# Kernel optimization log

Hardware: AMD Instinct MI355X
Metric: run time of the kernel (lower is better)

Reference implementation:

```python
import jax, jax.numpy as jnp
import numpy as np

N, E, H, NIN, DD = 10000, 160000, 128, 128, 256
SCALE = 30.0
EPS = 1e-5

def _ln(x, g, b):
    mu = jnp.mean(x, axis=-1, keepdims=True)
    var = jnp.mean((x - mu) ** 2, axis=-1, keepdims=True)
    return (x - mu) * jax.lax.rsqrt(var + EPS) * g + b

def _gelu(x):
    return jax.nn.gelu(x, approximate=False)  # torch nn.GELU default (erf)

def setup_inputs() -> dict:
    key = jax.random.key(0)
    ks = jax.random.split(key, 16)
    def w(k, i, o):
        return jax.random.normal(k, (i, o), jnp.float32) * (1.0 / np.sqrt(i))
    return {
        "h_V": jax.random.normal(ks[0], (N, H), jnp.float32),
        "h_E": jax.random.normal(ks[1], (E, H + NIN), jnp.float32),
        "edge_idx": jax.random.randint(ks[2], (2, E), 0, N, jnp.int32),
        # message MLP: (H+NIN)->H, H->H
        "m_w0": w(ks[3], H + NIN, H), "m_b0": jnp.zeros((H,), jnp.float32),
        "m_w1": w(ks[4], H, H),       "m_b1": jnp.zeros((H,), jnp.float32),
        # dense MLP: H->DD, DD->DD, final DD->H
        "d_w0": w(ks[5], H, DD),  "d_b0": jnp.zeros((DD,), jnp.float32),
        "d_w1": w(ks[6], DD, DD), "d_b1": jnp.zeros((DD,), jnp.float32),
        "d_w2": w(ks[7], DD, H),  "d_b2": jnp.zeros((H,), jnp.float32),
        # LayerNorm params
        "g1": jnp.ones((H,), jnp.float32), "be1": jnp.zeros((H,), jnp.float32),
        "g2": jnp.ones((H,), jnp.float32), "be2": jnp.zeros((H,), jnp.float32),
    }

def reference(h_V, h_E, edge_idx, m_w0, m_b0, m_w1, m_b1,
              d_w0, d_b0, d_w1, d_b1, d_w2, d_b2, g1, be1, g2, be2):
    src_idx = edge_idx[0]
    # message MLP over edges (dropout = identity at inference)
    h = _gelu(h_E @ m_w0 + m_b0)
    h_message = _gelu(h @ m_w1 + m_b1)          # [E, H]
    # scatter-sum aggregate edges -> nodes
    dh = jax.ops.segment_sum(h_message, src_idx, num_segments=N) / SCALE
    h_V = _ln(h_V + dh, g1, be1)
    # dense MLP over nodes
    d = _gelu(h_V @ d_w0 + d_b0)
    d = _gelu(d @ d_w1 + d_b1)
    dh = d @ d_w2 + d_b2
    return _ln(h_V + dh, g2, be2)
```

## Files before the change

### kernel.cpp

```cpp
#include <hip/hip_runtime.h>
#include <hip/hip_bf16.h>


typedef __attribute__((ext_vector_type(8))) short bf16x8;
typedef __attribute__((ext_vector_type(4))) float f32x4;

__device__ __forceinline__ unsigned short f2bf(float f) {
  union { float f; unsigned u; } v; v.f = f;
  return (unsigned short)((v.u + 0x7fffu + ((v.u >> 16) & 1u)) >> 16);
}
__device__ __forceinline__ unsigned pk2bf(float a, float b) {
  __hip_bfloat162 h = __float22bfloat162_rn(make_float2(a, b));
  union { __hip_bfloat162 h; unsigned u; } v; v.h = h;
  return v.u;
}
__device__ __forceinline__ float bf2f(unsigned s) {
  union { unsigned u; float f; } v; v.u = s << 16;
  return v.f;
}
__device__ __forceinline__ float gelu_f(float x) {
  float u = x * 0.70710678118654752f;
  float au = fabsf(u);
  float t = __builtin_amdgcn_rcpf(1.0f + 0.3275911f * au);
  float poly = ((((1.061405429f * t - 1.453152027f) * t + 1.421413741f) * t -
                 0.284496736f) * t + 0.254829592f) * t;
  float e = __expf(-au * au);
  float erfu = copysignf(1.0f - poly * e, u);
  return 0.5f * x * (1.0f + erfu);
}

__global__ void k_pack(const float* __restrict__ mw0, const float* __restrict__ mw1,
                       const float* __restrict__ dw0, const float* __restrict__ dw1,
                       const float* __restrict__ dw2,
                       unsigned short* __restrict__ pw0, unsigned short* __restrict__ pw1,
                       unsigned short* __restrict__ pd0, unsigned short* __restrict__ pd1,
                       unsigned short* __restrict__ pd2) {
  int g = blockIdx.x, lane = threadIdx.x;
  const float* src; unsigned short* dst; int K, N, WC, base;
  if (g < 64)       { src = mw0; dst = pw0; K = 256; N = 128; WC = 32; base = 0; }
  else if (g < 96)  { src = mw1; dst = pw1; K = 128; N = 128; WC = 32; base = 64; }
  else if (g < 160) { src = dw0; dst = pd0; K = 128; N = 256; WC = 64; base = 96; }
  else if (g < 288) { src = dw1; dst = pd1; K = 256; N = 256; WC = 32; base = 160; }
  else              { src = dw2; dst = pd2; K = 256; N = 128; WC = 32; base = 288; }
  int lg = g - base;
  int KS = K >> 5, CTKS = (WC >> 4) * KS;
  int w = lg / CTKS, rem = lg % CTKS, ct = rem / KS, ks = rem % KS;
  int col = w * WC + ct * 16 + (lane & 15);
  int k0 = ks * 32 + (lane >> 4) * 8;
  unsigned short o[8];
#pragma unroll
  for (int j = 0; j < 8; ++j) o[j] = f2bf(src[(size_t)(k0 + j) * N + col]);
  uint4 u;
  u.x = (unsigned)o[0] | ((unsigned)o[1] << 16);
  u.y = (unsigned)o[2] | ((unsigned)o[3] << 16);
  u.z = (unsigned)o[4] | ((unsigned)o[5] << 16);
  u.w = (unsigned)o[6] | ((unsigned)o[7] << 16);
  *(uint4*)(dst + (size_t)(lg * 64 + lane) * 8) = u;
}

__global__ void k_hist(const int* __restrict__ eidx, int* __restrict__ counts, int E) {
  int e = blockIdx.x * 256 + threadIdx.x;
  if (e < E) atomicAdd(&counts[eidx[e]], 1);
}

__global__ __launch_bounds__(1024) void k_scan(const int* __restrict__ counts,
                                               int* __restrict__ row_start,
                                               int* __restrict__ cursor, int Nn) {
  __shared__ int sm[1024];
  int t = threadIdx.x;
  int chunk = (Nn + 1023) / 1024;
  int lo = t * chunk, hi = lo + chunk;
  if (hi > Nn) hi = Nn;
  int s = 0;
  for (int i = lo; i < hi; ++i) s += counts[i];
  sm[t] = s;
  __syncthreads();
  for (int o = 1; o < 1024; o <<= 1) {
    int u = (t >= o) ? sm[t - o] : 0;
    __syncthreads();
    sm[t] += u;
    __syncthreads();
  }
  int run = sm[t] - s;
  for (int i = lo; i < hi; ++i) {
    row_start[i] = run; cursor[i] = run; run += counts[i];
  }
  if (t == 1023) row_start[Nn] = sm[1023];
}

__global__ void k_scatter(const int* __restrict__ eidx, int* __restrict__ cursor,
                          int* __restrict__ eorder, int E) {
  int e = blockIdx.x * 256 + threadIdx.x;
  if (e < E) {
    int pos = atomicAdd(&cursor[eidx[e]], 1);
    eorder[pos] = e;
  }
}

__global__ __launch_bounds__(256, 3) void k_edge(
    const float* __restrict__ hE, const unsigned short* __restrict__ pw0,
    const unsigned short* __restrict__ pw1, const float* __restrict__ b0,
    const float* __restrict__ b1, unsigned short* __restrict__ hmsg, int E) {
  __shared__ __align__(16) char ldsA[64 * 512];
  const int tid = threadIdx.x;
  const int wid = tid >> 6, lane = tid & 63;
  const int l15 = lane & 15, lhi = lane >> 4;
  const int wcol = wid * 32;

  bf16x8 B0[16], B1[8];
  {
    const uint4* p0 = (const uint4*)pw0 + (size_t)(wid * 16) * 64 + lane;
#pragma unroll
    for (int f = 0; f < 16; ++f) { uint4 v = p0[(size_t)f * 64]; B0[f] = *(bf16x8*)&v; }
    const uint4* p1 = (const uint4*)pw1 + (size_t)(wid * 8) * 64 + lane;
#pragma unroll
    for (int f = 0; f < 8; ++f) { uint4 v = p1[(size_t)f * 64]; B1[f] = *(bf16x8*)&v; }
  }
  float bb0[2], bb1[2];
#pragma unroll
  for (int ct = 0; ct < 2; ++ct) {
    bb0[ct] = b0[wcol + ct * 16 + l15];
    bb1[ct] = b1[wcol + ct * 16 + l15];
  }

  const int row0 = blockIdx.x << 6;
  const float4* src = (const float4*)hE + (size_t)row0 * 64;
#pragma unroll
  for (int p = 0; p < 16; ++p) {
    int idx = p * 256 + tid;
    int r = idx >> 6, c4 = idx & 63;
    float4 v = make_float4(0.f, 0.f, 0.f, 0.f);
    if (row0 + r < E) v = src[(size_t)r * 64 + c4];
    uint2 u;
    u.x = pk2bf(v.x, v.y);
    u.y = pk2bf(v.z, v.w);
    *(uint2*)(ldsA + r * 512 + ((c4 * 8) ^ ((r & 7) << 4))) = u;
  }
  __syncthreads();

  f32x4 acc[4][2];
#pragma unroll
  for (int mt = 0; mt < 4; ++mt)
#pragma unroll
    for (int ct = 0; ct < 2; ++ct) acc[mt][ct] = 0.f;
#pragma unroll
  for (int ks = 0; ks < 8; ++ks) {
    bf16x8 a[4];
#pragma unroll
    for (int mt = 0; mt < 4; ++mt) {
      int row = mt * 16 + l15;
      a[mt] = *(bf16x8*)(ldsA + row * 512 + ((ks * 64 + lhi * 16) ^ ((row & 7) << 4)));
    }
#pragma unroll
    for (int mt = 0; mt < 4; ++mt)
#pragma unroll
      for (int ct = 0; ct < 2; ++ct)
        acc[mt][ct] = __builtin_amdgcn_mfma_f32_16x16x32_bf16(a[mt], B0[ct * 8 + ks],
                                                             acc[mt][ct], 0, 0, 0);
  }
  __syncthreads();

#pragma unroll
  for (int mt = 0; mt < 4; ++mt)
#pragma unroll
    for (int ct = 0; ct < 2; ++ct)
#pragma unroll
      for (int j = 0; j < 4; ++j) {
        int r = mt * 16 + lhi * 4 + j;
        int col = wcol + ct * 16 + l15;
        float g = gelu_f(acc[mt][ct][j] + bb0[ct]);
        *(unsigned short*)(ldsA + r * 256 + ((col * 2) ^ ((r & 7) << 4))) = f2bf(g);
      }
  __syncthreads();

  f32x4 acc2[4][2];
#pragma unroll
  for (int mt = 0; mt < 4; ++mt)
#pragma unroll
    for (int ct = 0; ct < 2; ++ct) acc2[mt][ct] = 0.f;
#pragma unroll
  for (int ks = 0; ks < 4; ++ks) {
    bf16x8 a[4];
#pragma unroll
    for (int mt = 0; mt < 4; ++mt) {
      int row = mt * 16 + l15;
      a[mt] = *(bf16x8*)(ldsA + row * 256 + ((ks * 64 + lhi * 16) ^ ((row & 7) << 4)));
    }
#pragma unroll
    for (int mt = 0; mt < 4; ++mt)
#pragma unroll
      for (int ct = 0; ct < 2; ++ct)
        acc2[mt][ct] = __builtin_amdgcn_mfma_f32_16x16x32_bf16(a[mt], B1[ct * 4 + ks],
                                                              acc2[mt][ct], 0, 0, 0);
  }
#pragma unroll
  for (int mt = 0; mt < 4; ++mt)
#pragma unroll
    for (int ct = 0; ct < 2; ++ct)
#pragma unroll
      for (int j = 0; j < 4; ++j) {
        int r = mt * 16 + lhi * 4 + j;
        if (row0 + r < E) {
          int col = wcol + ct * 16 + l15;
          hmsg[(size_t)(row0 + r) * 128 + col] = f2bf(gelu_f(acc2[mt][ct][j] + bb1[ct]));
        }
      }
}

__global__ __launch_bounds__(256) void k_aggln(
    const unsigned* __restrict__ hmsg, const float2* __restrict__ hV,
    const int* __restrict__ row_start, const int* __restrict__ eorder,
    const float* __restrict__ g1, const float* __restrict__ be1,
    float2* __restrict__ hv1f, unsigned* __restrict__ hv1b, int Nn) {
  int wid = threadIdx.x >> 6, lane = threadIdx.x & 63;
  int node = blockIdx.x * 4 + wid;
  if (node >= Nn) return;
  int s = row_start[node], e = row_start[node + 1];
  float s0 = 0.f, s1 = 0.f;
  int i = s;
  for (; i + 3 < e; i += 4) {
    int e0 = eorder[i], e1 = eorder[i + 1], e2 = eorder[i + 2], e3 = eorder[i + 3];
    unsigned v0 = hmsg[(size_t)e0 * 64 + lane];
    unsigned v1 = hmsg[(size_t)e1 * 64 + lane];
    unsigned v2 = hmsg[(size_t)e2 * 64 + lane];
    unsigned v3 = hmsg[(size_t)e3 * 64 + lane];
    s0 += bf2f(v0 & 0xffffu) + bf2f(v1 & 0xffffu) + bf2f(v2 & 0xffffu) + bf2f(v3 & 0xffffu);
    s1 += bf2f(v0 >> 16) + bf2f(v1 >> 16) + bf2f(v2 >> 16) + bf2f(v3 >> 16);
  }
  for (; i < e; ++i) {
    unsigned v = hmsg[(size_t)eorder[i] * 64 + lane];
    s0 += bf2f(v & 0xffffu);
    s1 += bf2f(v >> 16);
  }
  float2 hv = hV[(size_t)node * 64 + lane];
  float x0 = hv.x + s0 * (1.f / 30.f);
  float x1 = hv.y + s1 * (1.f / 30.f);
  float sum = x0 + x1, sq = x0 * x0 + x1 * x1;
#pragma unroll
  for (int off = 32; off > 0; off >>= 1) {
    sum += __shfl_xor(sum, off);
    sq += __shfl_xor(sq, off);
  }
  float mu = sum * (1.f / 128.f);
  float var = sq * (1.f / 128.f) - mu * mu;
  float rs = rsqrtf(var + 1e-5f);
  int c = lane * 2;
  float y0 = (x0 - mu) * rs * g1[c] + be1[c];
  float y1 = (x1 - mu) * rs * g1[c + 1] + be1[c + 1];
  hv1f[(size_t)node * 64 + lane] = make_float2(y0, y1);
  hv1b[(size_t)node * 64 + lane] = (unsigned)f2bf(y0) | ((unsigned)f2bf(y1) << 16);
}

__global__ __launch_bounds__(256) void k_d0(const unsigned short* __restrict__ xb,
                                            const unsigned short* __restrict__ pd0,
                                            const float* __restrict__ bias,
                                            unsigned short* __restrict__ out, int Nn) {
  __shared__ __align__(16) char ldsA[64 * 256];
  const int tid = threadIdx.x, wid = tid >> 6, lane = tid & 63;
  const int l15 = lane & 15, lhi = lane >> 4;
  const int row0 = blockIdx.x * 64;
#pragma unroll
  for (int p = 0; p < 4; ++p) {
    int idx = p * 256 + tid;
    int r = idx >> 4, c = idx & 15;
    uint4 v = make_uint4(0u, 0u, 0u, 0u);
    if (row0 + r < Nn) v = ((const uint4*)xb)[(size_t)(row0 + r) * 16 + c];
    *(uint4*)(ldsA + r * 256 + ((c * 16) ^ ((r & 7) << 4))) = v;
  }
  bf16x8 B[16];
  {
    const uint4* p0 = (const uint4*)pd0 + (size_t)(wid * 16) * 64 + lane;
#pragma unroll
    for (int f = 0; f < 16; ++f) { uint4 v = p0[(size_t)f * 64]; B[f] = *(bf16x8*)&v; }
  }
  __syncthreads();
  f32x4 acc[4][4];
#pragma unroll
  for (int mt = 0; mt < 4; ++mt)
#pragma unroll
    for (int ct = 0; ct < 4; ++ct) acc[mt][ct] = 0.f;
#pragma unroll
  for (int ks = 0; ks < 4; ++ks) {
    bf16x8 a[4];
#pragma unroll
    for (int mt = 0; mt < 4; ++mt) {
      int row = mt * 16 + l15;
      a[mt] = *(bf16x8*)(ldsA + row * 256 + ((ks * 64 + lhi * 16) ^ ((row & 7) << 4)));
    }
#pragma unroll
    for (int mt = 0; mt < 4; ++mt)
#pragma unroll
      for (int ct = 0; ct < 4; ++ct)
        acc[mt][ct] = __builtin_amdgcn_mfma_f32_16x16x32_bf16(a[mt], B[ct * 4 + ks],
                                                             acc[mt][ct], 0, 0, 0);
  }
  float bb[4];
#pragma unroll
  for (int ct = 0; ct < 4; ++ct) bb[ct] = bias[wid * 64 + ct * 16 + l15];
#pragma unroll
  for (int mt = 0; mt < 4; ++mt)
#pragma unroll
    for (int ct = 0; ct < 4; ++ct)
#pragma unroll
      for (int j = 0; j < 4; ++j) {
        int r = row0 + mt * 16 + lhi * 4 + j;
        if (r < Nn) {
          int col = wid * 64 + ct * 16 + l15;
          out[(size_t)r * 256 + col] = f2bf(gelu_f(acc[mt][ct][j] + bb[ct]));
        }
      }
}

__global__ __launch_bounds__(512) void k_d1(const unsigned short* __restrict__ d0,
                                            const unsigned short* __restrict__ pd1,
                                            const float* __restrict__ bias,
                                            unsigned short* __restrict__ out, int Nn) {
  __shared__ __align__(16) char ldsA[64 * 512];
  const int tid = threadIdx.x, wid = tid >> 6, lane = tid & 63;
  const int l15 = lane & 15, lhi = lane >> 4;
  const int wcol = wid * 32;
  const int row0 = blockIdx.x * 64;
#pragma unroll
  for (int p = 0; p < 4; ++p) {
    int idx = p * 512 + tid;
    int r = idx >> 5, c = idx & 31;
    uint4 v = make_uint4(0u, 0u, 0u, 0u);
    if (row0 + r < Nn) v = ((const uint4*)d0)[(size_t)(row0 + r) * 32 + c];
    *(uint4*)(ldsA + r * 512 + ((c * 16) ^ ((r & 7) << 4))) = v;
  }
  bf16x8 B[16];
  {
    const uint4* p0 = (const uint4*)pd1 + (size_t)(wid * 16) * 64 + lane;
#pragma unroll
    for (int f = 0; f < 16; ++f) { uint4 v = p0[(size_t)f * 64]; B[f] = *(bf16x8*)&v; }
  }
  __syncthreads();
  f32x4 acc[4][2];
#pragma unroll
  for (int mt = 0; mt < 4; ++mt)
#pragma unroll
    for (int ct = 0; ct < 2; ++ct) acc[mt][ct] = 0.f;
#pragma unroll
  for (int ks = 0; ks < 8; ++ks) {
    bf16x8 a[4];
#pragma unroll
    for (int mt = 0; mt < 4; ++mt) {
      int row = mt * 16 + l15;
      a[mt] = *(bf16x8*)(ldsA + row * 512 + ((ks * 64 + lhi * 16) ^ ((row & 7) << 4)));
    }
#pragma unroll
    for (int mt = 0; mt < 4; ++mt)
#pragma unroll
      for (int ct = 0; ct < 2; ++ct)
        acc[mt][ct] = __builtin_amdgcn_mfma_f32_16x16x32_bf16(a[mt], B[ct * 8 + ks],
                                                             acc[mt][ct], 0, 0, 0);
  }
  float bb[2];
#pragma unroll
  for (int ct = 0; ct < 2; ++ct) bb[ct] = bias[wcol + ct * 16 + l15];
#pragma unroll
  for (int mt = 0; mt < 4; ++mt)
#pragma unroll
    for (int ct = 0; ct < 2; ++ct)
#pragma unroll
      for (int j = 0; j < 4; ++j) {
        int r = row0 + mt * 16 + lhi * 4 + j;
        if (r < Nn) {
          int col = wcol + ct * 16 + l15;
          out[(size_t)r * 256 + col] = f2bf(gelu_f(acc[mt][ct][j] + bb[ct]));
        }
      }
}

__global__ __launch_bounds__(256) void k_d2(const unsigned short* __restrict__ d1,
                                            const unsigned short* __restrict__ pd2,
                                            const float* __restrict__ bias,
                                            const float* __restrict__ hv1f,
                                            const float* __restrict__ g2,
                                            const float* __restrict__ be2,
                                            float* __restrict__ out, int Nn) {
  __shared__ __align__(16) char ldsA[64 * 512];
  const int tid = threadIdx.x, wid = tid >> 6, lane = tid & 63;
  const int l15 = lane & 15, lhi = lane >> 4;
  const int wcol = wid * 32;
  const int row0 = blockIdx.x * 64;
#pragma unroll
  for (int p = 0; p < 8; ++p) {
    int idx = p * 256 + tid;
    int r = idx >> 5, c = idx & 31;
    uint4 v = make_uint4(0u, 0u, 0u, 0u);
    if (row0 + r < Nn) v = ((const uint4*)d1)[(size_t)(row0 + r) * 32 + c];
    *(uint4*)(ldsA + r * 512 + ((c * 16) ^ ((r & 7) << 4))) = v;
  }
  bf16x8 B[16];
  {
    const uint4* p0 = (const uint4*)pd2 + (size_t)(wid * 16) * 64 + lane;
#pragma unroll
    for (int f = 0; f < 16; ++f) { uint4 v = p0[(size_t)f * 64]; B[f] = *(bf16x8*)&v; }
  }
  __syncthreads();
  f32x4 acc[4][2];
#pragma unroll
  for (int mt = 0; mt < 4; ++mt)
#pragma unroll
    for (int ct = 0; ct < 2; ++ct) acc[mt][ct] = 0.f;
#pragma unroll
  for (int ks = 0; ks < 8; ++ks) {
    bf16x8 a[4];
#pragma unroll
    for (int mt = 0; mt < 4; ++mt) {
      int row = mt * 16 + l15;
      a[mt] = *(bf16x8*)(ldsA + row * 512 + ((ks * 64 + lhi * 16) ^ ((row & 7) << 4)));
    }
#pragma unroll
    for (int mt = 0; mt < 4; ++mt)
#pragma unroll
      for (int ct = 0; ct < 2; ++ct)
        acc[mt][ct] = __builtin_amdgcn_mfma_f32_16x16x32_bf16(a[mt], B[ct * 8 + ks],
                                                             acc[mt][ct], 0, 0, 0);
  }
  float bb[2];
#pragma unroll
  for (int ct = 0; ct < 2; ++ct) bb[ct] = bias[wcol + ct * 16 + l15];
  __syncthreads();
  float* yl = (float*)ldsA;
#pragma unroll
  for (int mt = 0; mt < 4; ++mt)
#pragma unroll
    for (int ct = 0; ct < 2; ++ct)
#pragma unroll
      for (int j = 0; j < 4; ++j) {
        int r = mt * 16 + lhi * 4 + j;
        int grow = row0 + r;
        int col = wcol + ct * 16 + l15;
        float res = (grow < Nn) ? hv1f[(size_t)grow * 128 + col] : 0.f;
        yl[r * 128 + col] = acc[mt][ct][j] + bb[ct] + res;
      }
  __syncthreads();
  float g2a = g2[lane * 2], g2b = g2[lane * 2 + 1];
  float ba = be2[lane * 2], bbx = be2[lane * 2 + 1];
  for (int ii = 0; ii < 16; ++ii) {
    int r = wid * 16 + ii;
    int grow = row0 + r;
    if (grow >= Nn) continue;
    float2 xy = *(float2*)&yl[r * 128 + lane * 2];
    float sum = xy.x + xy.y, sq = xy.x * xy.x + xy.y * xy.y;
#pragma unroll
    for (int off = 32; off > 0; off >>= 1) {
      sum += __shfl_xor(sum, off);
      sq += __shfl_xor(sq, off);
    }
    float mu = sum * (1.f / 128.f);
    float var = sq * (1.f / 128.f) - mu * mu;
    float rs = rsqrtf(var + 1e-5f);
    float y0 = (xy.x - mu) * rs * g2a + ba;
    float y1 = (xy.y - mu) * rs * g2b + bbx;
    *(float2*)&out[(size_t)grow * 128 + lane * 2] = make_float2(y0, y1);
  }
}

extern "C" void kernel_launch(void* const* d_in, const int* in_sizes, int n_in,
                              void* d_out, int out_size, void* d_ws, size_t ws_size,
                              hipStream_t stream) {
  const float* hV  = (const float*)d_in[0];
  const float* hE  = (const float*)d_in[1];
  const int* eidx  = (const int*)d_in[2];
  const float* mw0 = (const float*)d_in[3];
  const float* mb0 = (const float*)d_in[4];
  const float* mw1 = (const float*)d_in[5];
  const float* mb1 = (const float*)d_in[6];
  const float* dw0 = (const float*)d_in[7];
  const float* db0 = (const float*)d_in[8];
  const float* dw1 = (const float*)d_in[9];
  const float* db1 = (const float*)d_in[10];
  const float* dw2 = (const float*)d_in[11];
  const float* db2 = (const float*)d_in[12];
  const float* g1  = (const float*)d_in[13];
  const float* be1 = (const float*)d_in[14];
  const float* g2  = (const float*)d_in[15];
  const float* be2 = (const float*)d_in[16];
  const int Nn = in_sizes[0] / 128;
  const int E  = in_sizes[1] / 256;

  char* ws = (char*)d_ws;
  size_t off = 0;
  auto alloc = [&](size_t bytes) -> char* {
    off = (off + 255) & ~(size_t)255;
    char* p = ws + off;
    off += bytes;
    return p;
  };
  unsigned short* hmsg = (unsigned short*)alloc((size_t)E * 128 * 2);
  float* hv1f          = (float*)alloc((size_t)Nn * 128 * 4);
  unsigned short* hv1b = (unsigned short*)alloc((size_t)Nn * 128 * 2);
  unsigned short* d0b  = (unsigned short*)alloc((size_t)Nn * 256 * 2);
  unsigned short* d1b  = (unsigned short*)alloc((size_t)Nn * 256 * 2);
  unsigned short* pw0  = (unsigned short*)alloc(32768 * 2);
  unsigned short* pw1  = (unsigned short*)alloc(16384 * 2);
  unsigned short* pd0  = (unsigned short*)alloc(32768 * 2);
  unsigned short* pd1  = (unsigned short*)alloc(65536 * 2);
  unsigned short* pd2  = (unsigned short*)alloc(32768 * 2);
  int* counts    = (int*)alloc((size_t)Nn * 4);
  int* row_start = (int*)alloc((size_t)(Nn + 1) * 4);
  int* cursor    = (int*)alloc((size_t)Nn * 4);
  int* eorder    = (int*)alloc((size_t)E * 4);

  hipMemsetAsync(counts, 0, (size_t)Nn * 4, stream);
  k_pack<<<352, 64, 0, stream>>>(mw0, mw1, dw0, dw1, dw2, pw0, pw1, pd0, pd1, pd2);
  k_hist<<<(E + 255) / 256, 256, 0, stream>>>(eidx, counts, E);
  k_scan<<<1, 1024, 0, stream>>>(counts, row_start, cursor, Nn);
  k_scatter<<<(E + 255) / 256, 256, 0, stream>>>(eidx, cursor, eorder, E);
  const int etiles = (E + 63) / 64;
  k_edge<<<etiles, 256, 0, stream>>>(hE, pw0, pw1, mb0, mb1, hmsg, E);
  k_aggln<<<(Nn + 3) / 4, 256, 0, stream>>>((const unsigned*)hmsg, (const float2*)hV,
                                            row_start, eorder, g1, be1,
                                            (float2*)hv1f, (unsigned*)hv1b, Nn);
  const int nt = (Nn + 63) / 64;
  k_d0<<<nt, 256, 0, stream>>>(hv1b, pd0, db0, d0b, Nn);
  k_d1<<<nt, 512, 0, stream>>>(d0b, pd1, db1, d1b, Nn);
  k_d2<<<nt, 256, 0, stream>>>(d1b, pd2, db2, hv1f, g2, be2, (float*)d_out, Nn);
}
```

Before: 160.1 us.

## Persistent double-buffered edge MLP with direct-to-LDS loads; fuse node MLP kernels

The edge MLP becomes a persistent kernel over 32-row tiles. It stages fp32 h_E rows straight into double-buffered LDS with global_load_lds, so the next tile's load overlaps the current tile's MFMA work, and it converts to bf16 when reading fragments. The three dense node-MLP kernels are merged into one k_node kernel that keeps the intermediate activations in LDS instead of writing them to global memory and reading them back. The trade-offs are lower occupancy in k_edge (launch bounds 2, larger LDS), per-k-step streaming of weights from global in k_node, and k_node running only 157 blocks at occupancy 1.

```diff
diff --git a/kernel.cpp b/kernel.cpp
--- a/kernel.cpp
+++ b/kernel.cpp
@@ -27,6 +27,11 @@
   float e = __expf(-au * au);
   float erfu = copysignf(1.0f - poly * e, u);
   return 0.5f * x * (1.0f + erfu);
+}
+
+__device__ __forceinline__ void gl2lds16(const void* g, void* l) {
+  __builtin_amdgcn_global_load_lds((const __attribute__((address_space(1))) unsigned*)g,
+                                   (__attribute__((address_space(3))) unsigned*)l, 16, 0, 0);
 }
 
 __global__ void k_pack(const float* __restrict__ mw0, const float* __restrict__ mw1,
@@ -40,7 +45,7 @@
   if (g < 64)       { src = mw0; dst = pw0; K = 256; N = 128; WC = 32; base = 0; }
   else if (g < 96)  { src = mw1; dst = pw1; K = 128; N = 128; WC = 32; base = 64; }
   else if (g < 160) { src = dw0; dst = pd0; K = 128; N = 256; WC = 64; base = 96; }
-  else if (g < 288) { src = dw1; dst = pd1; K = 256; N = 256; WC = 32; base = 160; }
+  else if (g < 288) { src = dw1; dst = pd1; K = 256; N = 256; WC = 64; base = 160; }
   else              { src = dw2; dst = pd2; K = 256; N = 128; WC = 32; base = 288; }
   int lg = g - base;
   int KS = K >> 5, CTKS = (WC >> 4) * KS;
@@ -97,11 +102,14 @@
   }
 }
 
-__global__ __launch_bounds__(256, 3) void k_edge(
+#define AST 1040
+#define ABUF 33280
+__global__ __launch_bounds__(256, 2) void k_edge(
     const float* __restrict__ hE, const unsigned short* __restrict__ pw0,
     const unsigned short* __restrict__ pw1, const float* __restrict__ b0,
     const float* __restrict__ b1, unsigned short* __restrict__ hmsg, int E) {
-  __shared__ __align__(16) char ldsA[64 * 512];
+  __shared__ __align__(16) char lds[2 * ABUF + 8192];
+  char* Hb = lds + 2 * ABUF;
   const int tid = threadIdx.x;
   const int wid = tid >> 6, lane = tid & 63;
   const int l15 = lane & 15, lhi = lane >> 4;
@@ -122,89 +130,113 @@
     bb0[ct] = b0[wcol + ct * 16 + l15];
     bb1[ct] = b1[wcol + ct * 16 + l15];
   }
-
-  const int row0 = blockIdx.x << 6;
-  const float4* src = (const float4*)hE + (size_t)row0 * 64;
-#pragma unroll
-  for (int p = 0; p < 16; ++p) {
-    int idx = p * 256 + tid;
-    int r = idx >> 6, c4 = idx & 63;
-    float4 v = make_float4(0.f, 0.f, 0.f, 0.f);
-    if (row0 + r < E) v = src[(size_t)r * 64 + c4];
-    uint2 u;
-    u.x = pk2bf(v.x, v.y);
-    u.y = pk2bf(v.z, v.w);
-    *(uint2*)(ldsA + r * 512 + ((c4 * 8) ^ ((r & 7) << 4))) = u;
-  }
   __syncthreads();
 
-  f32x4 acc[4][2];
-#pragma unroll
-  for (int mt = 0; mt < 4; ++mt)
-#pragma unroll
-    for (int ct = 0; ct < 2; ++ct) acc[mt][ct] = 0.f;
-#pragma unroll
-  for (int ks = 0; ks < 8; ++ks) {
-    bf16x8 a[4];
-#pragma unroll
-    for (int mt = 0; mt < 4; ++mt) {
-      int row = mt * 16 + l15;
-      a[mt] = *(bf16x8*)(ldsA + row * 512 + ((ks * 64 + lhi * 16) ^ ((row & 7) << 4)));
-    }
-#pragma unroll
-    for (int mt = 0; mt < 4; ++mt)
+  const int TILES = (E + 31) >> 5;
+  auto STAGE = [&](int tile, int buf) {
+    char* dstb = lds + buf * ABUF + (wid * 8) * AST;
+#pragma unroll
+    for (int i = 0; i < 8; ++i) {
+      int grow = tile * 32 + wid * 8 + i;
+      grow = grow < E ? grow : E - 1;
+      const float* g = hE + (size_t)grow * 256 + lane * 4;
+      gl2lds16(g, dstb + i * AST);
+    }
+  };
+
+  int t = blockIdx.x;
+  int cur = 0;
+  if (t < TILES) STAGE(t, 0);
+  for (; t < TILES; t += gridDim.x) {
+    int tn = t + gridDim.x;
+    if (tn < TILES) {
+      STAGE(tn, cur ^ 1);
+      asm volatile("s_waitcnt vmcnt(8)" ::: "memory");
+    } else {
+      asm volatile("s_waitcnt vmcnt(0)" ::: "memory");
+    }
+    __builtin_amdgcn_s_barrier();
+    __builtin_amdgcn_sched_barrier(0);
+
+    const char* A = lds + cur * ABUF;
+    f32x4 acc[2][2];
+#pragma unroll
+    for (int mt = 0; mt < 2; ++mt)
+#pragma unroll
+      for (int ct = 0; ct < 2; ++ct) acc[mt][ct] = 0.f;
+#pragma unroll
+    for (int ks = 0; ks < 8; ++ks) {
+      bf16x8 a[2];
+#pragma unroll
+      for (int mt = 0; mt < 2; ++mt) {
+        int row = mt * 16 + l15;
+        const char* p = A + row * AST + ks * 128 + lhi * 32;
+        f32x4 lo = *(const f32x4*)p;
+        f32x4 hi = *(const f32x4*)(p + 16);
+        union { unsigned u[4]; bf16x8 v; } pk;
+        pk.u[0] = pk2bf(lo[0], lo[1]);
+        pk.u[1] = pk2bf(lo[2], lo[3]);
+        pk.u[2] = pk2bf(hi[0], hi[1]);
+        pk.u[3] = pk2bf(hi[2], hi[3]);
+        a[mt] = pk.v;
+      }
+#pragma unroll
+      for (int mt = 0; mt < 2; ++mt)
+#pragma unroll
+        for (int ct = 0; ct < 2; ++ct)
+          acc[mt][ct] = __builtin_amdgcn_mfma_f32_16x16x32_bf16(a[mt], B0[ct * 8 + ks],
+                                                               acc[mt][ct], 0, 0, 0);
+    }
+#pragma unroll
+    for (int mt = 0; mt < 2; ++mt)
 #pragma unroll
       for (int ct = 0; ct < 2; ++ct)
-        acc[mt][ct] = __builtin_amdgcn_mfma_f32_16x16x32_bf16(a[mt], B0[ct * 8 + ks],
-                                                             acc[mt][ct], 0, 0, 0);
-  }
-  __syncthreads();
-
-#pragma unroll
-  for (int mt = 0; mt < 4; ++mt)
-#pragma unroll
-    for (int ct = 0; ct < 2; ++ct)
-#pragma unroll
-      for (int j = 0; j < 4; ++j) {
-        int r = mt * 16 + lhi * 4 + j;
-        int col = wcol + ct * 16 + l15;
-        float g = gelu_f(acc[mt][ct][j] + bb0[ct]);
-        *(unsigned short*)(ldsA + r * 256 + ((col * 2) ^ ((r & 7) << 4))) = f2bf(g);
-      }
-  __syncthreads();
-
-  f32x4 acc2[4][2];
-#pragma unroll
-  for (int mt = 0; mt < 4; ++mt)
-#pragma unroll
-    for (int ct = 0; ct < 2; ++ct) acc2[mt][ct] = 0.f;
-#pragma unroll
-  for (int ks = 0; ks < 4; ++ks) {
-    bf16x8 a[4];
-#pragma unroll
-    for (int mt = 0; mt < 4; ++mt) {
-      int row = mt * 16 + l15;
-      a[mt] = *(bf16x8*)(ldsA + row * 256 + ((ks * 64 + lhi * 16) ^ ((row & 7) << 4)));
-    }
-#pragma unroll
-    for (int mt = 0; mt < 4; ++mt)
+#pragma unroll
+        for (int j = 0; j < 4; ++j) {
+          int r = mt * 16 + lhi * 4 + j;
+          int col = wcol + ct * 16 + l15;
+          float g = gelu_f(acc[mt][ct][j] + bb0[ct]);
+          *(unsigned short*)(Hb + r * 256 + ((col * 2) ^ ((r & 7) << 4))) = f2bf(g);
+        }
+    asm volatile("s_waitcnt lgkmcnt(0)" ::: "memory");
+    __builtin_amdgcn_s_barrier();
+    __builtin_amdgcn_sched_barrier(0);
+
+    f32x4 acc2[2][2];
+#pragma unroll
+    for (int mt = 0; mt < 2; ++mt)
+#pragma unroll
+      for (int ct = 0; ct < 2; ++ct) acc2[mt][ct] = 0.f;
+#pragma unroll
+    for (int ks = 0; ks < 4; ++ks) {
+      bf16x8 a[2];
+#pragma unroll
+      for (int mt = 0; mt < 2; ++mt) {
+        int row = mt * 16 + l15;
+        a[mt] = *(bf16x8*)(Hb + row * 256 + ((ks * 64 + lhi * 16) ^ ((row & 7) << 4)));
+      }
+#pragma unroll
+      for (int mt = 0; mt < 2; ++mt)
+#pragma unroll
+        for (int ct = 0; ct < 2; ++ct)
+          acc2[mt][ct] = __builtin_amdgcn_mfma_f32_16x16x32_bf16(a[mt], B1[ct * 4 + ks],
+                                                                acc2[mt][ct], 0, 0, 0);
+    }
+    const int row0 = t * 32;
+#pragma unroll
+    for (int mt = 0; mt < 2; ++mt)
 #pragma unroll
       for (int ct = 0; ct < 2; ++ct)
-        acc2[mt][ct] = __builtin_amdgcn_mfma_f32_16x16x32_bf16(a[mt], B1[ct * 4 + ks],
-                                                              acc2[mt][ct], 0, 0, 0);
-  }
-#pragma unroll
-  for (int mt = 0; mt < 4; ++mt)
-#pragma unroll
-    for (int ct = 0; ct < 2; ++ct)
-#pragma unroll
-      for (int j = 0; j < 4; ++j) {
-        int r = mt * 16 + lhi * 4 + j;
-        if (row0 + r < E) {
-          int col = wcol + ct * 16 + l15;
-          hmsg[(size_t)(row0 + r) * 128 + col] = f2bf(gelu_f(acc2[mt][ct][j] + bb1[ct]));
+#pragma unroll
+        for (int j = 0; j < 4; ++j) {
+          int r = row0 + mt * 16 + lhi * 4 + j;
+          if (r < E) {
+            int col = wcol + ct * 16 + l15;
+            hmsg[(size_t)r * 128 + col] = f2bf(gelu_f(acc2[mt][ct][j] + bb1[ct]));
+          }
         }
-      }
+    cur ^= 1;
+  }
 }
 
 __global__ __launch_bounds__(256) void k_aggln(
@@ -251,199 +283,158 @@
   hv1b[(size_t)node * 64 + lane] = (unsigned)f2bf(y0) | ((unsigned)f2bf(y1) << 16);
 }
 
-__global__ __launch_bounds__(256) void k_d0(const unsigned short* __restrict__ xb,
-                                            const unsigned short* __restrict__ pd0,
-                                            const float* __restrict__ bias,
-                                            unsigned short* __restrict__ out, int Nn) {
-  __shared__ __align__(16) char ldsA[64 * 256];
+__global__ __launch_bounds__(256, 1) void k_node(
+    const unsigned short* __restrict__ xb, const unsigned short* __restrict__ pd0,
+    const unsigned short* __restrict__ pd1, const unsigned short* __restrict__ pd2,
+    const float* __restrict__ db0, const float* __restrict__ db1,
+    const float* __restrict__ db2, const float* __restrict__ hv1f,
+    const float* __restrict__ g2, const float* __restrict__ be2,
+    float* __restrict__ out, int Nn) {
+  __shared__ __align__(16) char lds[16384 + 32768 + 32768];
+  char* A0 = lds;
+  char* D0 = lds + 16384;
+  char* D1 = lds + 16384 + 32768;
+  float* Y = (float*)D0;
   const int tid = threadIdx.x, wid = tid >> 6, lane = tid & 63;
   const int l15 = lane & 15, lhi = lane >> 4;
   const int row0 = blockIdx.x * 64;
+
 #pragma unroll
   for (int p = 0; p < 4; ++p) {
     int idx = p * 256 + tid;
     int r = idx >> 4, c = idx & 15;
     uint4 v = make_uint4(0u, 0u, 0u, 0u);
     if (row0 + r < Nn) v = ((const uint4*)xb)[(size_t)(row0 + r) * 16 + c];
-    *(uint4*)(ldsA + r * 256 + ((c * 16) ^ ((r & 7) << 4))) = v;
-  }
-  bf16x8 B[16];
+    *(uint4*)(A0 + r * 256 + ((c * 16) ^ ((r & 7) << 4))) = v;
+  }
+  __syncthreads();
+
   {
-    const uint4* p0 = (const uint4*)pd0 + (size_t)(wid * 16) * 64 + lane;
-#pragma unroll
-    for (int f = 0; f < 16; ++f) { uint4 v = p0[(size_t)f * 64]; B[f] = *(bf16x8*)&v; }
+    f32x4 acc[4][4];
+#pragma unroll
+    for (int mt = 0; mt < 4; ++mt)
+#pragma unroll
+      for (int ct = 0; ct < 4; ++ct) acc[mt][ct] = 0.f;
+#pragma unroll
+    for (int ks = 0; ks < 4; ++ks) {
+      bf16x8 a[4];
+#pragma unroll
+      for (int mt = 0; mt < 4; ++mt) {
+        int row = mt * 16 + l15;
+        a[mt] = *(bf16x8*)(A0 + row * 256 + ((ks * 64 + lhi * 16) ^ ((row & 7) << 4)));
+      }
+#pragma unroll
+      for (int ct = 0; ct < 4; ++ct) {
+        uint4 bv = ((const uint4*)pd0)[(size_t)(wid * 16 + ct * 4 + ks) * 64 + lane];
+        bf16x8 b = *(bf16x8*)&bv;
+#pragma unroll
+        for (int mt = 0; mt < 4; ++mt)
+          acc[mt][ct] = __builtin_amdgcn_mfma_f32_16x16x32_bf16(a[mt], b, acc[mt][ct], 0, 0, 0);
+      }
+    }
+#pragma unroll
+    for (int ct = 0; ct < 4; ++ct) {
+      float bb = db0[wid * 64 + ct * 16 + l15];
+      int col = wid * 64 + ct * 16 + l15;
+#pragma unroll
+      for (int mt = 0; mt < 4; ++mt)
+#pragma unroll
+        for (int j = 0; j < 4; ++j) {
+          int r = mt * 16 + lhi * 4 + j;
+          *(unsigned short*)(D0 + r * 512 + ((col * 2) ^ ((r & 7) << 4))) =
+              f2bf(gelu_f(acc[mt][ct][j] + bb));
+        }
+    }
   }
   __syncthreads();
-  f32x4 acc[4][4];
-#pragma unroll
-  for (int mt = 0; mt < 4; ++mt)
-#pragma unroll
-    for (int ct = 0; ct < 4; ++ct) acc[mt][ct] = 0.f;
-#pragma unroll
-  for (int ks = 0; ks < 4; ++ks) {
-    bf16x8 a[4];
-#pragma unroll
-    for (int mt = 0; mt < 4; ++mt) {
-      int row = mt * 16 + l15;
-      a[mt] = *(bf16x8*)(ldsA + row * 256 + ((ks * 64 + lhi * 16) ^ ((row & 7) << 4)));
-    }
+
+  {
+    f32x4 acc[4][4];
 #pragma unroll
     for (int mt = 0; mt < 4; ++mt)
 #pragma unroll
-      for (int ct = 0; ct < 4; ++ct)
-        acc[mt][ct] = __builtin_amdgcn_mfma_f32_16x16x32_bf16(a[mt], B[ct * 4 + ks],
-                                                             acc[mt][ct], 0, 0, 0);
-  }
-  float bb[4];
-#pragma unroll
-  for (int ct = 0; ct < 4; ++ct) bb[ct] = bias[wid * 64 + ct * 16 + l15];
-#pragma unroll
-  for (int mt = 0; mt < 4; ++mt)
-#pragma unroll
-    for (int ct = 0; ct < 4; ++ct)
-#pragma unroll
-      for (int j = 0; j < 4; ++j) {
-        int r = row0 + mt * 16 + lhi * 4 + j;
-        if (r < Nn) {
-          int col = wid * 64 + ct * 16 + l15;
-          out[(size_t)r * 256 + col] = f2bf(gelu_f(acc[mt][ct][j] + bb[ct]));
+      for (int ct = 0; ct < 4; ++ct) acc[mt][ct] = 0.f;
+#pragma unroll
+    for (int ks = 0; ks < 8; ++ks) {
+      bf16x8 a[4];
+#pragma unroll
+      for (int mt = 0; mt < 4; ++mt) {
+        int row = mt * 16 + l15;
+        a[mt] = *(bf16x8*)(D0 + row * 512 + ((ks * 64 + lhi * 16) ^ ((row & 7) << 4)));
+      }
+#pragma unroll
+      for (int ct = 0; ct < 4; ++ct) {
+        uint4 bv = ((const uint4*)pd1)[(size_t)(wid * 32 + ct * 8 + ks) * 64 + lane];
+        bf16x8 b = *(bf16x8*)&bv;
+#pragma unroll
+        for (int mt = 0; mt < 4; ++mt)
+          acc[mt][ct] = __builtin_amdgcn_mfma_f32_16x16x32_bf16(a[mt], b, acc[mt][ct], 0, 0, 0);
+      }
+    }
+#pragma unroll
+    for (int ct = 0; ct < 4; ++ct) {
+      float bb = db1[wid * 64 + ct * 16 + l15];
+      int col = wid * 64 + ct * 16 + l15;
+#pragma unroll
+      for (int mt = 0; mt < 4; ++mt)
+#pragma unroll
+        for (int j = 0; j < 4; ++j) {
+          int r = mt * 16 + lhi * 4 + j;
+          *(unsigned short*)(D1 + r * 512 + ((col * 2) ^ ((r & 7) << 4))) =
+              f2bf(gelu_f(acc[mt][ct][j] + bb));
         }
-      }
-}
-
-__global__ __launch_bounds__(512) void k_d1(const unsigned short* __restrict__ d0,
-                                            const unsigned short* __restrict__ pd1,
-                                            const float* __restrict__ bias,
-                                            unsigned short* __restrict__ out, int Nn) {
-  __shared__ __align__(16) char ldsA[64 * 512];
-  const int tid = threadIdx.x, wid = tid >> 6, lane = tid & 63;
-  const int l15 = lane & 15, lhi = lane >> 4;
-  const int wcol = wid * 32;
-  const int row0 = blockIdx.x * 64;
-#pragma unroll
-  for (int p = 0; p < 4; ++p) {
-    int idx = p * 512 + tid;
-    int r = idx >> 5, c = idx & 31;
-    uint4 v = make_uint4(0u, 0u, 0u, 0u);
-    if (row0 + r < Nn) v = ((const uint4*)d0)[(size_t)(row0 + r) * 32 + c];
-    *(uint4*)(ldsA + r * 512 + ((c * 16) ^ ((r & 7) << 4))) = v;
-  }
-  bf16x8 B[16];
+    }
+  }
+  __syncthreads();
+
   {
-    const uint4* p0 = (const uint4*)pd1 + (size_t)(wid * 16) * 64 + lane;
-#pragma unroll
-    for (int f = 0; f < 16; ++f) { uint4 v = p0[(size_t)f * 64]; B[f] = *(bf16x8*)&v; }
+    f32x4 acc[4][2];
+#pragma unroll
+    for (int mt = 0; mt < 4; ++mt)
+#pragma unroll
+      for (int ct = 0; ct < 2; ++ct) acc[mt][ct] = 0.f;
+#pragma unroll
+    for (int ks = 0; ks < 8; ++ks) {
+      bf16x8 a[4];
+#pragma unroll
+      for (int mt = 0; mt < 4; ++mt) {
+        int row = mt * 16 + l15;
+        a[mt] = *(bf16x8*)(D1 + row * 512 + ((ks * 64 + lhi * 16) ^ ((row & 7) << 4)));
+      }
+#pragma unroll
+      for (int ct = 0; ct < 2; ++ct) {
+        uint4 bv = ((const uint4*)pd2)[(size_t)(wid * 16 + ct * 8 + ks) * 64 + lane];
+        bf16x8 b = *(bf16x8*)&bv;
+#pragma unroll
+        for (int mt = 0; mt < 4; ++mt)
+          acc[mt][ct] = __builtin_amdgcn_mfma_f32_16x16x32_bf16(a[mt], b, acc[mt][ct], 0, 0, 0);
+      }
+    }
+    __syncthreads();
+#pragma unroll
+    for (int ct = 0; ct < 2; ++ct) {
+      float bb = db2[wid * 32 + ct * 16 + l15];
+      int col = wid * 32 + ct * 16 + l15;
+#pragma unroll
+      for (int mt = 0; mt < 4; ++mt)
+#pragma unroll
+        for (int j = 0; j < 4; ++j) {
+          int r = mt * 16 + lhi * 4 + j;
+          int grow = row0 + r;
+          float res = (grow < Nn) ? hv1f[(size_t)grow * 128 + col] : 0.f;
+          Y[r * 128 + col] = acc[mt][ct][j] + bb + res;
+        }
+    }
   }
   __syncthreads();
-  f32x4 acc[4][2];
-#pragma unroll
-  for (int mt = 0; mt < 4; ++mt)
-#pragma unroll
-    for (int ct = 0; ct < 2; ++ct) acc[mt][ct] = 0.f;
-#pragma unroll
-  for (int ks = 0; ks < 8; ++ks) {
-    bf16x8 a[4];
-#pragma unroll
-    for (int mt = 0; mt < 4; ++mt) {
-      int row = mt * 16 + l15;
-      a[mt] = *(bf16x8*)(ldsA + row * 512 + ((ks * 64 + lhi * 16) ^ ((row & 7) << 4)));
-    }
-#pragma unroll
-    for (int mt = 0; mt < 4; ++mt)
-#pragma unroll
-      for (int ct = 0; ct < 2; ++ct)
-        acc[mt][ct] = __builtin_amdgcn_mfma_f32_16x16x32_bf16(a[mt], B[ct * 8 + ks],
-                                                             acc[mt][ct], 0, 0, 0);
-  }
-  float bb[2];
-#pragma unroll
-  for (int ct = 0; ct < 2; ++ct) bb[ct] = bias[wcol + ct * 16 + l15];
-#pragma unroll
-  for (int mt = 0; mt < 4; ++mt)
-#pragma unroll
-    for (int ct = 0; ct < 2; ++ct)
-#pragma unroll
-      for (int j = 0; j < 4; ++j) {
-        int r = row0 + mt * 16 + lhi * 4 + j;
-        if (r < Nn) {
-          int col = wcol + ct * 16 + l15;
-          out[(size_t)r * 256 + col] = f2bf(gelu_f(acc[mt][ct][j] + bb[ct]));
-        }
-      }
-}
-
-__global__ __launch_bounds__(256) void k_d2(const unsigned short* __restrict__ d1,
-                                            const unsigned short* __restrict__ pd2,
-                                            const float* __restrict__ bias,
-                                            const float* __restrict__ hv1f,
-                                            const float* __restrict__ g2,
-                                            const float* __restrict__ be2,
-                                            float* __restrict__ out, int Nn) {
-  __shared__ __align__(16) char ldsA[64 * 512];
-  const int tid = threadIdx.x, wid = tid >> 6, lane = tid & 63;
-  const int l15 = lane & 15, lhi = lane >> 4;
-  const int wcol = wid * 32;
-  const int row0 = blockIdx.x * 64;
-#pragma unroll
-  for (int p = 0; p < 8; ++p) {
-    int idx = p * 256 + tid;
-    int r = idx >> 5, c = idx & 31;
-    uint4 v = make_uint4(0u, 0u, 0u, 0u);
-    if (row0 + r < Nn) v = ((const uint4*)d1)[(size_t)(row0 + r) * 32 + c];
-    *(uint4*)(ldsA + r * 512 + ((c * 16) ^ ((r & 7) << 4))) = v;
-  }
-  bf16x8 B[16];
-  {
-    const uint4* p0 = (const uint4*)pd2 + (size_t)(wid * 16) * 64 + lane;
-#pragma unroll
-    for (int f = 0; f < 16; ++f) { uint4 v = p0[(size_t)f * 64]; B[f] = *(bf16x8*)&v; }
-  }
-  __syncthreads();
-  f32x4 acc[4][2];
-#pragma unroll
-  for (int mt = 0; mt < 4; ++mt)
-#pragma unroll
-    for (int ct = 0; ct < 2; ++ct) acc[mt][ct] = 0.f;
-#pragma unroll
-  for (int ks = 0; ks < 8; ++ks) {
-    bf16x8 a[4];
-#pragma unroll
-    for (int mt = 0; mt < 4; ++mt) {
-      int row = mt * 16 + l15;
-      a[mt] = *(bf16x8*)(ldsA + row * 512 + ((ks * 64 + lhi * 16) ^ ((row & 7) << 4)));
-    }
-#pragma unroll
-    for (int mt = 0; mt < 4; ++mt)
-#pragma unroll
-      for (int ct = 0; ct < 2; ++ct)
-        acc[mt][ct] = __builtin_amdgcn_mfma_f32_16x16x32_bf16(a[mt], B[ct * 8 + ks],
-                                                             acc[mt][ct], 0, 0, 0);
-  }
-  float bb[2];
-#pragma unroll
-  for (int ct = 0; ct < 2; ++ct) bb[ct] = bias[wcol + ct * 16 + l15];
-  __syncthreads();
-  float* yl = (float*)ldsA;
-#pragma unroll
-  for (int mt = 0; mt < 4; ++mt)
-#pragma unroll
-    for (int ct = 0; ct < 2; ++ct)
-#pragma unroll
-      for (int j = 0; j < 4; ++j) {
-        int r = mt * 16 + lhi * 4 + j;
-        int grow = row0 + r;
-        int col = wcol + ct * 16 + l15;
-        float res = (grow < Nn) ? hv1f[(size_t)grow * 128 + col] : 0.f;
-        yl[r * 128 + col] = acc[mt][ct][j] + bb[ct] + res;
-      }
-  __syncthreads();
+
   float g2a = g2[lane * 2], g2b = g2[lane * 2 + 1];
   float ba = be2[lane * 2], bbx = be2[lane * 2 + 1];
   for (int ii = 0; ii < 16; ++ii) {
     int r = wid * 16 + ii;
     int grow = row0 + r;
     if (grow >= Nn) continue;
-    float2 xy = *(float2*)&yl[r * 128 + lane * 2];
+    float2 xy = *(float2*)&Y[r * 128 + lane * 2];
     float sum = xy.x + xy.y, sq = xy.x * xy.x + xy.y * xy.y;
 #pragma unroll
     for (int off = 32; off > 0; off >>= 1) {
@@ -493,8 +484,6 @@
   unsigned short* hmsg = (unsigned short*)alloc((size_t)E * 128 * 2);
   float* hv1f          = (float*)alloc((size_t)Nn * 128 * 4);
   unsigned short* hv1b = (unsigned short*)alloc((size_t)Nn * 128 * 2);
-  unsigned short* d0b  = (unsigned short*)alloc((size_t)Nn * 256 * 2);
-  unsigned short* d1b  = (unsigned short*)alloc((size_t)Nn * 256 * 2);
   unsigned short* pw0  = (unsigned short*)alloc(32768 * 2);
   unsigned short* pw1  = (unsigned short*)alloc(16384 * 2);
   unsigned short* pd0  = (unsigned short*)alloc(32768 * 2);
@@ -510,13 +499,11 @@
   k_hist<<<(E + 255) / 256, 256, 0, stream>>>(eidx, counts, E);
   k_scan<<<1, 1024, 0, stream>>>(counts, row_start, cursor, Nn);
   k_scatter<<<(E + 255) / 256, 256, 0, stream>>>(eidx, cursor, eorder, E);
-  const int etiles = (E + 63) / 64;
-  k_edge<<<etiles, 256, 0, stream>>>(hE, pw0, pw1, mb0, mb1, hmsg, E);
+  k_edge<<<512, 256, 0, stream>>>(hE, pw0, pw1, mb0, mb1, hmsg, E);
   k_aggln<<<(Nn + 3) / 4, 256, 0, stream>>>((const unsigned*)hmsg, (const float2*)hV,
                                             row_start, eorder, g1, be1,
                                             (float2*)hv1f, (unsigned*)hv1b, Nn);
   const int nt = (Nn + 63) / 64;
-  k_d0<<<nt, 256, 0, stream>>>(hv1b, pd0, db0, d0b, Nn);
-  k_d1<<<nt, 512, 0, stream>>>(d0b, pd1, db1, d1b, Nn);
-  k_d2<<<nt, 256, 0, stream>>>(d1b, pd2, db2, hv1f, g2, be2, (float*)d_out, Nn);
-}
+  k_node<<<nt, 256, 0, stream>>>(hv1b, pd0, pd1, pd2, db0, db1, db2,
+                                 hv1f, g2, be2, (float*)d_out, Nn);
+}
```

After: 144.5 us. 1.11x faster.
